# Kernel tuning notes

Measured on AMD Instinct MI355X. Metric: run time of the kernel, lower is better.

## Reference

```python
import jax, jax.numpy as jnp
import numpy as np
from jax import lax

DIM = 192
HEADS = 4
EPS = 1e-12  # torch F.normalize eps


def setup_inputs() -> dict:
    key = jax.random.key(0)
    ks = jax.random.split(key, 8)
    b, c, h, w = 2, DIM, 64, 64
    x = jax.random.normal(ks[0], (b, c, h, w), dtype=jnp.float32)
    # 1x1 qkv conv: weight [3c, c], bias [3c]
    w_qkv = jax.random.normal(ks[1], (3 * c, c), dtype=jnp.float32) * 0.05
    b_qkv = jax.random.normal(ks[2], (3 * c,), dtype=jnp.float32) * 0.05
    # 3x3 depthwise conv (groups = 3c): weight [3c, 1, 3, 3], bias [3c]
    w_dw = jax.random.normal(ks[3], (3 * c, 1, 3, 3), dtype=jnp.float32) * 0.05
    b_dw = jax.random.normal(ks[4], (3 * c,), dtype=jnp.float32) * 0.05
    # 1x1 output projection: weight [c, c], bias [c]
    w_proj = jax.random.normal(ks[5], (c, c), dtype=jnp.float32) * 0.05
    b_proj = jax.random.normal(ks[6], (c,), dtype=jnp.float32) * 0.05
    temperature = jnp.ones((HEADS, 1, 1), dtype=jnp.float32)
    return {"x": x, "w_qkv": w_qkv, "b_qkv": b_qkv, "w_dw": w_dw,
            "b_dw": b_dw, "w_proj": w_proj, "b_proj": b_proj,
            "temperature": temperature}


def _l2norm(t, axis):
    n = jnp.sqrt(jnp.sum(t * t, axis=axis, keepdims=True))
    return t / jnp.maximum(n, EPS)


def reference(x, w_qkv, b_qkv, w_dw, b_dw, w_proj, b_proj, temperature):
    b, c, h, w = x.shape
    heads = temperature.shape[0]
    hd = c // heads  # head dim
    # 1x1 conv -> [b, 3c, h, w]
    qkv = jnp.einsum('bchw,oc->bohw', x, w_qkv) + b_qkv[None, :, None, None]
    # 3x3 depthwise conv, padding 1
    qkv = lax.conv_general_dilated(
        qkv, w_dw, window_strides=(1, 1), padding=((1, 1), (1, 1)),
        dimension_numbers=('NCHW', 'OIHW', 'NCHW'),
        feature_group_count=3 * c) + b_dw[None, :, None, None]
    q, k, v = jnp.split(qkv, 3, axis=1)
    # [b, heads, hd, n] with n = h*w
    q = q.reshape(b, heads, hd, h * w)
    k = k.reshape(b, heads, hd, h * w)
    v = v.reshape(b, heads, hd, h * w)
    q = _l2norm(q, axis=2)
    k = _l2norm(k, axis=2)
    # spatial cosine attention: [b, heads, n, n]
    attn = jnp.einsum('bhdn,bhdm->bhnm', q, k) * temperature[None]
    attn = jax.nn.softmax(attn, axis=-1)
    # out[b,h,d,n] = sum_m attn[n,m] * v[d,m]
    out = jnp.einsum('bhnm,bhdm->bhdn', attn, v)
    out = out.reshape(b, c, h, w)
    out = jnp.einsum('bchw,oc->bohw', out, w_proj) + b_proj[None, :, None, None]
    return out
```

## Files before the change

kernel.cpp:

```cpp
#include <hip/hip_runtime.h>
#include <hip/hip_bf16.h>


#define BB 2
#define CCH 192
#define C3 576
#define NH 4
#define HD 48
#define NP 4096

typedef __hip_bfloat16 bf16;
typedef __attribute__((ext_vector_type(8))) short bf16x8;
typedef __attribute__((ext_vector_type(4))) float f32x4;

union I4B8 { int4 i; bf16x8 v; };

__device__ inline float bf2f(bf16 v){ return __bfloat162float(v); }
__device__ inline unsigned short bfbits(bf16 v){ return __builtin_bit_cast(unsigned short, v); }
__device__ inline unsigned short f2bfbits(float f){ return __builtin_bit_cast(unsigned short, __float2bfloat16(f)); }
__device__ inline float bfb2f(short s){ return __uint_as_float(((unsigned)(unsigned short)s)<<16); }

__global__ void probe_kernel(const unsigned* __restrict__ x, int* __restrict__ flag)
{
  int t = threadIdx.x;
  unsigned u = x[t];
  int e = (u >> 7) & 0xff;
  int sane = (e >= 100 && e <= 140) || ((u & 0x7fffu) == 0u);
  __shared__ int cnt;
  if (t == 0) cnt = 0;
  __syncthreads();
  if (sane) atomicAdd(&cnt, 1);
  __syncthreads();
  if (t == 0) *flag = (cnt >= 192) ? 1 : 0;
}

#define NCANON 153988
__global__ __launch_bounds__(256) void convert_params_kernel(
    const int* __restrict__ flag,
    const void* w_qkv, const void* b_qkv, const void* w_dw, const void* b_dw,
    const void* w_proj, const void* b_proj, const void* temp,
    bf16* __restrict__ canon)
{
  const bool isbf = (*flag != 0);
  int i = blockIdx.x*256 + threadIdx.x;
  if (i >= NCANON) return;
  const void* src; int off;
  if      (i < 110592){ src = w_qkv;  off = i; }
  else if (i < 111168){ src = b_qkv;  off = i - 110592; }
  else if (i < 116352){ src = w_dw;   off = i - 111168; }
  else if (i < 116928){ src = b_dw;   off = i - 116352; }
  else if (i < 153792){ src = w_proj; off = i - 116928; }
  else if (i < 153984){ src = b_proj; off = i - 153792; }
  else                { src = temp;   off = i - 153984; }
  float v = isbf ? bf2f(((const bf16*)src)[off]) : ((const float*)src)[off];
  canon[i] = __float2bfloat16(v);
}

__global__ __launch_bounds__(256) void transpose_x_kernel(
    const int* __restrict__ flag, const void* __restrict__ Xv,
    short* __restrict__ XT)
{
  const bool isbf = (*flag != 0);
  __shared__ short T[64][66];
  const int c0 = blockIdx.x*64, p0 = blockIdx.y*64, b = blockIdx.z;
  const size_t xbase = (size_t)b*CCH*NP;
  #pragma unroll
  for (int s=0;s<16;s++){
    int i = threadIdx.x + s*256;
    int cc = i>>6, pp = i&63;
    size_t g = xbase + (size_t)(c0+cc)*NP + p0+pp;
    float v = isbf ? bf2f(((const bf16*)Xv)[g]) : ((const float*)Xv)[g];
    T[cc][pp] = (short)f2bfbits(v);
  }
  __syncthreads();
  #pragma unroll
  for (int s=0;s<16;s++){
    int i = threadIdx.x + s*256;
    int pl = i>>6, cl = i&63;
    XT[((size_t)b*NP + p0+pl)*CCH + c0+cl] = T[cl][pl];
  }
}

__global__ __launch_bounds__(256) void conv1x1_mfma_kernel(
    const int* __restrict__ flag, int ydyn,
    const short* __restrict__ XT,
    const bf16* __restrict__ Wt,
    const bf16* __restrict__ bias,
    void* __restrict__ Yv, int OC)
{
  const bool yf32 = ydyn && (*flag == 0);
  __shared__ __align__(16) short Bs[2][128*32];
  const int tid = threadIdx.x, wave = tid>>6, lane = tid&63;
  const int l16 = lane&15, quad = lane>>4;
  const int o0 = blockIdx.x*64, p0 = blockIdx.y*128, b = blockIdx.z;
  const short* XTb = XT + ((size_t)b*NP + p0)*CCH;
  const short* Wb  = (const short*)Wt;

  f32x4 acc[4][2];
  #pragma unroll
  for (int mt=0;mt<4;mt++){
    #pragma unroll
    for (int r=0;r<4;r++){
      float bv = bf2f(bias[o0+mt*16+quad*4+r]);
      acc[mt][0][r]=bv; acc[mt][1][r]=bv;
    }
  }

  int4 sreg[2];
  I4B8 Afr[2][4];
  #define CLOAD(kc) { _Pragma("unroll") for (int s_=0;s_<2;s_++){ int i_=tid+256*s_; \
      sreg[s_] = *(const int4*)&XTb[(size_t)(i_>>2)*CCH + (kc)*32 + (i_&3)*8]; } }
  #define CSTORE(buf) { _Pragma("unroll") for (int s_=0;s_<2;s_++){ int i_=tid+256*s_; \
      *(int4*)&Bs[buf][(i_>>2)*32 + (i_&3)*8] = sreg[s_]; } }
  #define ALOAD(kc, buf) { _Pragma("unroll") for (int mt_=0;mt_<4;mt_++){ \
      Afr[buf][mt_].i = *(const int4*)&Wb[(size_t)(o0+mt_*16+l16)*CCH + (kc)*32 + quad*8]; } }

  CLOAD(0); CSTORE(0); ALOAD(0,0);
  __syncthreads();

  #pragma unroll
  for (int kc=0; kc<6; kc++){
    const int cur = kc&1;
    if (kc<5){ CLOAD(kc+1); ALOAD(kc+1, cur^1); }
    I4B8 Bf0, Bf1;
    Bf0.i = *(const int4*)&Bs[cur][(wave*32 + l16)*32 + quad*8];
    Bf1.i = *(const int4*)&Bs[cur][(wave*32 + 16 + l16)*32 + quad*8];
    #pragma unroll
    for (int mt=0;mt<4;mt++){
      acc[mt][0] = __builtin_amdgcn_mfma_f32_16x16x32_bf16(Afr[cur][mt].v, Bf0.v, acc[mt][0], 0,0,0);
      acc[mt][1] = __builtin_amdgcn_mfma_f32_16x16x32_bf16(Afr[cur][mt].v, Bf1.v, acc[mt][1], 0,0,0);
    }
    if (kc<5) CSTORE(cur^1);
    __syncthreads();
  }
  #undef CLOAD
  #undef CSTORE
  #undef ALOAD

  #pragma unroll
  for (int mt=0;mt<4;mt++)
    #pragma unroll
    for (int nt=0;nt<2;nt++)
      #pragma unroll
      for (int r=0;r<4;r++){
        int o = o0 + mt*16 + quad*4 + r;
        int p = p0 + wave*32 + nt*16 + l16;
        size_t off = ((size_t)b*OC + o)*NP + p;
        if (yf32) ((float*)Yv)[off] = acc[mt][nt][r];
        else      ((bf16*)Yv)[off]  = __float2bfloat16(acc[mt][nt][r]);
      }
}

__global__ __launch_bounds__(256) void dwconv_kernel(
    const bf16* __restrict__ in, const bf16* __restrict__ w,
    const bf16* __restrict__ bias, bf16* __restrict__ out)
{
  __shared__ __align__(16) short img[4096];
  const int bc = blockIdx.x; const int ch = bc % C3;
  const int tid = threadIdx.x;
  const int4* g4 = (const int4*)(in + (size_t)bc*NP);
  int4* s4 = (int4*)img;
  s4[tid] = g4[tid];
  s4[tid+256] = g4[tid+256];
  float wv[9];
  #pragma unroll
  for (int j=0;j<9;j++) wv[j] = bf2f(w[ch*9+j]);
  const float bv = bf2f(bias[ch]);
  __syncthreads();

  const int y = tid>>2, x0 = (tid&3)*16;
  unsigned outw[8];
  #pragma unroll
  for (int j=0;j<16;j++){
    int x = x0+j;
    float s = bv;
    #pragma unroll
    for (int ky=0;ky<3;ky++){
      int yy = y+ky-1; if (yy<0||yy>63) continue;
      const short* rp = &img[yy<<6];
      #pragma unroll
      for (int kx=0;kx<3;kx++){
        int xx = x+kx-1; if (xx<0||xx>63) continue;
        s += wv[ky*3+kx]*bfb2f(rp[xx]);
      }
    }
    unsigned hb = f2bfbits(s);
    if (j&1) outw[j>>1] |= hb<<16; else outw[j>>1] = hb;
  }
  int4* op = (int4*)((short*)out + (size_t)bc*NP + (y<<6) + x0);
  op[0] = *(int4*)&outw[0];
  op[1] = *(int4*)&outw[4];
}

__global__ __launch_bounds__(256) void l2norm_t_kernel(
    bf16* __restrict__ buf, short* __restrict__ KT)
{
  int idx = blockIdx.x*256 + threadIdx.x;
  int n = idx & 4095; int t = idx >> 12;
  int head = t & 3; int qk = (t>>2)&1; int b = t>>3;
  bf16* p = buf + ((size_t)b*C3 + qk*CCH + head*HD)*NP + n;
  float v[HD];
  float ss = 0.f;
  #pragma unroll
  for (int d=0; d<HD; d++){ v[d] = bf2f(p[(size_t)d*NP]); ss += v[d]*v[d]; }
  float inv = 1.0f / fmaxf(sqrtf(ss), 1e-12f);
  if (qk == 0){
    #pragma unroll
    for (int d=0; d<HD; d++) p[(size_t)d*NP] = __float2bfloat16(v[d]*inv);
  } else {
    short* row = KT + ((size_t)(b*NH+head)*NP + n)*64;
    int sw = n & 7;
    #pragma unroll
    for (int u=0; u<8; u++){
      int4 w = {0,0,0,0};
      if (u < 6){
        int d0 = u*8;
        w.x = (unsigned)f2bfbits(v[d0+0]*inv) | ((unsigned)f2bfbits(v[d0+1]*inv)<<16);
        w.y = (unsigned)f2bfbits(v[d0+2]*inv) | ((unsigned)f2bfbits(v[d0+3]*inv)<<16);
        w.z = (unsigned)f2bfbits(v[d0+4]*inv) | ((unsigned)f2bfbits(v[d0+5]*inv)<<16);
        w.w = (unsigned)f2bfbits(v[d0+6]*inv) | ((unsigned)f2bfbits(v[d0+7]*inv)<<16);
      }
      *(int4*)&row[(u^sw)*8] = w;
    }
  }
}

__global__ __launch_bounds__(256) void flash_kernel(
    const bf16* __restrict__ qkv,
    const short* __restrict__ KT,
    const bf16* __restrict__ temp,
    short* __restrict__ OT)
{
  __shared__ __align__(16) short Ks[2][128*64];
  __shared__ __align__(16) short Vs[2][48*136];
  __shared__ __align__(16) short Ps[4][16*136];

  const int bh = blockIdx.x, b = bh>>2, head = bh&3;
  const int q0 = blockIdx.y * 64;
  const int tid = threadIdx.x, wave = tid>>6, lane = tid&63;
  const int l16 = lane&15, quad = lane>>4;

  const unsigned short* Qp = (const unsigned short*)(qkv + ((size_t)b*C3 + head*HD)*NP)
                             + q0 + wave*16 + l16;
  const short* Vp = (const short*)(qkv + ((size_t)b*C3 + 2*CCH + head*HD)*NP);
  const short* KTs = KT + (size_t)bh*NP*64;
  const float sc = bf2f(temp[head]) * 1.44269504f;
  const float negM = -__builtin_fabsf(sc);

  I4B8 A0, A1;
  {
    unsigned q0b[8];
    #pragma unroll
    for (int j=0;j<8;j++) q0b[j] = Qp[(size_t)(quad*8+j)*NP];
    A0.i.x = q0b[0] | (q0b[1]<<16); A0.i.y = q0b[2] | (q0b[3]<<16);
    A0.i.z = q0b[4] | (q0b[5]<<16); A0.i.w = q0b[6] | (q0b[7]<<16);
    if (quad < 2){
      unsigned q1b[8];
      #pragma unroll
      for (int j=0;j<8;j++) q1b[j] = Qp[(size_t)(32+quad*8+j)*NP];
      A1.i.x = q1b[0] | (q1b[1]<<16); A1.i.y = q1b[2] | (q1b[3]<<16);
      A1.i.z = q1b[4] | (q1b[5]<<16); A1.i.w = q1b[6] | (q1b[7]<<16);
    } else {
      A1.i.x = 0; A1.i.y = 0; A1.i.z = 0; A1.i.w = 0;
    }
  }

  f32x4 O0 = {0,0,0,0}, O1 = {0,0,0,0}, O2 = {0,0,0,0};
  float rs[4] = {0.f, 0.f, 0.f, 0.f};
  short* Pw = Ps[wave];
  const int sw = l16 & 7;

  int4 kreg[4], vreg[3];
  #define KLOAD(CHUNK) { const int k0_=(CHUNK)<<7; \
    const int4* gk_ = (const int4*)(KTs + (size_t)k0_*64); \
    _Pragma("unroll") for (int s_=0;s_<4;s_++) kreg[s_] = gk_[tid + 256*s_]; \
    _Pragma("unroll") for (int s_=0;s_<3;s_++){ int i_=tid+256*s_; \
      vreg[s_] = *(const int4*)(Vp + (size_t)(i_>>4)*NP + k0_ + (i_&15)*8); } }
  #define KSTORE(BUFI) { int4* lk_ = (int4*)&Ks[BUFI][0]; \
    _Pragma("unroll") for (int s_=0;s_<4;s_++) lk_[tid+256*s_] = kreg[s_]; \
    _Pragma("unroll") for (int s_=0;s_<3;s_++){ int i_=tid+256*s_; \
      *(int4*)&Vs[BUFI][(i_>>4)*136 + (i_&15)*8] = vreg[s_]; } }

  KLOAD(0); KSTORE(0);
  __syncthreads();

  for (int t=0; t<32; ++t){
    const int cur = t & 1;
    if (t < 31) KLOAD(t+1);

    const short* Kb = &Ks[cur][0];
    const short* Vb = &Vs[cur][0];

    f32x4 S[8];
    #pragma unroll
    for (int ct=0; ct<8; ++ct){
      const int row = (ct*16 + l16)*64;
      I4B8 B0, B1;
      B0.i = *(const int4*)&Kb[row + ((quad^sw)*8)];
      B1.i = *(const int4*)&Kb[row + (((4+quad)^sw)*8)];
      f32x4 z = {0,0,0,0};
      z = __builtin_amdgcn_mfma_f32_16x16x32_bf16(A0.v, B0.v, z, 0,0,0);
      z = __builtin_amdgcn_mfma_f32_16x16x32_bf16(A1.v, B1.v, z, 0,0,0);
      S[ct] = z;
    }

    #pragma unroll
    for (int r=0;r<4;r++){
      float acc0 = 0.f, acc1 = 0.f;
      #pragma unroll
      for (int ct=0;ct<8;ct++){
        float p = __builtin_amdgcn_exp2f(__builtin_fmaf(S[ct][r], sc, negM));
        if (ct & 1) acc1 += p; else acc0 += p;
        Pw[(quad*4+r)*136 + ct*16 + l16] = (short)f2bfbits(p);
      }
      rs[r] += acc0 + acc1;
    }

    #pragma unroll
    for (int c=0;c<4;c++){
      I4B8 AP, BV0, BV1, BV2;
      AP.i  = *(const int4*)&Pw[l16*136 + c*32 + quad*8];
      BV0.i = *(const int4*)&Vb[(l16   )*136 + c*32 + quad*8];
      BV1.i = *(const int4*)&Vb[(16+l16)*136 + c*32 + quad*8];
      BV2.i = *(const int4*)&Vb[(32+l16)*136 + c*32 + quad*8];
      O0 = __builtin_amdgcn_mfma_f32_16x16x32_bf16(AP.v, BV0.v, O0, 0,0,0);
      O1 = __builtin_amdgcn_mfma_f32_16x16x32_bf16(AP.v, BV1.v, O1, 0,0,0);
      O2 = __builtin_amdgcn_mfma_f32_16x16x32_bf16(AP.v, BV2.v, O2, 0,0,0);
    }

    if (t < 31) KSTORE(cur^1);
    __syncthreads();
  }
  #undef KLOAD
  #undef KSTORE

  float l[4];
  #pragma unroll
  for (int r=0;r<4;r++){
    float v = rs[r];
    v += __shfl_xor(v,1);
    v += __shfl_xor(v,2);
    v += __shfl_xor(v,4);
    v += __shfl_xor(v,8);
    l[r] = v;
  }

  #pragma unroll
  for (int r=0;r<4;r++){
    float invl = 1.0f / l[r];
    short* row = OT + ((size_t)b*NP + q0 + wave*16 + quad*4 + r)*CCH + head*HD;
    row[l16]    = (short)f2bfbits(O0[r]*invl);
    row[16+l16] = (short)f2bfbits(O1[r]*invl);
    row[32+l16] = (short)f2bfbits(O2[r]*invl);
  }
}

extern "C" void kernel_launch(void* const* d_in, const int* in_sizes, int n_in,
                              void* d_out, int out_size, void* d_ws, size_t ws_size,
                              hipStream_t stream)
{
  int*  flag  = (int*)d_ws;
  bf16* canon = (bf16*)((char*)d_ws + 16);
  bf16* bufA  = (bf16*)((char*)d_ws + 308096);
  bf16* bufB  = (bf16*)((char*)d_ws + 9745280);
  short* XT = (short*)bufB;
  short* OT = (short*)bufA;
  short* KT = (short*)(bufA + 1572864);

  bf16* cw_qkv  = canon;
  bf16* cb_qkv  = canon + 110592;
  bf16* cw_dw   = canon + 111168;
  bf16* cb_dw   = canon + 116352;
  bf16* cw_proj = canon + 116928;
  bf16* cb_proj = canon + 153792;
  bf16* ctemp   = canon + 153984;

  probe_kernel<<<1, 256, 0, stream>>>((const unsigned*)d_in[0], flag);
  convert_params_kernel<<<602, 256, 0, stream>>>(flag,
      d_in[1], d_in[2], d_in[3], d_in[4], d_in[5], d_in[6], d_in[7], canon);
  transpose_x_kernel<<<dim3(3,64,2), 256, 0, stream>>>(flag, d_in[0], XT);
  conv1x1_mfma_kernel<<<dim3(9,32,2), 256, 0, stream>>>(flag, 0,
      XT, cw_qkv, cb_qkv, bufA, C3);
  dwconv_kernel<<<dim3(BB*C3), 256, 0, stream>>>(bufA, cw_dw, cb_dw, bufB);
  l2norm_t_kernel<<<dim3(256), 256, 0, stream>>>(bufB, KT);
  flash_kernel<<<dim3(8,64), 256, 0, stream>>>(bufB, KT, ctemp, OT);
  conv1x1_mfma_kernel<<<dim3(3,32,2), 256, 0, stream>>>(flag, 1,
      OT, cw_proj, cb_proj, d_out, CCH);
}
```

Before: 205.4 us.

## Split attention over key range, keep P in registers, fuse probe into pre-pass

Merges the probe, parameter conversion and x transpose into a single pre-pass kernel that detects the input dtype per block with a wave ballot. The flash kernel is restructured: it computes S transposed (K as A operand), so P stays in registers instead of going through shared memory. It drops double-buffered K/V shared memory, allowing four blocks per CU. When the workspace is large enough it also splits the key range across two blocks and merges fp32 partial outputs and row sums in the projection kernel. This raises the grid from 512 to 1024 blocks to improve occupancy, at the cost of extra fp32 partial-output traffic and added syncs per iteration.

After: 263.9 us. 28.5% more time.

```diff
diff --git a/kernel.cpp b/kernel.cpp
--- a/kernel.cpp
+++ b/kernel.cpp
@@ -19,76 +19,66 @@
 __device__ inline unsigned short bfbits(bf16 v){ return __builtin_bit_cast(unsigned short, v); }
 __device__ inline unsigned short f2bfbits(float f){ return __builtin_bit_cast(unsigned short, __float2bfloat16(f)); }
 __device__ inline float bfb2f(short s){ return __uint_as_float(((unsigned)(unsigned short)s)<<16); }
-
-__global__ void probe_kernel(const unsigned* __restrict__ x, int* __restrict__ flag)
-{
-  int t = threadIdx.x;
-  unsigned u = x[t];
+__device__ inline unsigned pk2(float a, float b){
+  return (unsigned)f2bfbits(a) | ((unsigned)f2bfbits(b)<<16);
+}
+
+__device__ inline bool probe64(const void* x){
+  unsigned u = ((const unsigned*)x)[threadIdx.x & 63];
   int e = (u >> 7) & 0xff;
   int sane = (e >= 100 && e <= 140) || ((u & 0x7fffu) == 0u);
-  __shared__ int cnt;
-  if (t == 0) cnt = 0;
-  __syncthreads();
-  if (sane) atomicAdd(&cnt, 1);
-  __syncthreads();
-  if (t == 0) *flag = (cnt >= 192) ? 1 : 0;
+  unsigned long long m = __ballot(sane);
+  return __popcll(m) >= 48;
 }
 
 #define NCANON 153988
-__global__ __launch_bounds__(256) void convert_params_kernel(
-    const int* __restrict__ flag,
+__global__ __launch_bounds__(256) void pre_kernel(
+    const void* __restrict__ Xv,
     const void* w_qkv, const void* b_qkv, const void* w_dw, const void* b_dw,
     const void* w_proj, const void* b_proj, const void* temp,
-    bf16* __restrict__ canon)
-{
-  const bool isbf = (*flag != 0);
-  int i = blockIdx.x*256 + threadIdx.x;
-  if (i >= NCANON) return;
-  const void* src; int off;
-  if      (i < 110592){ src = w_qkv;  off = i; }
-  else if (i < 111168){ src = b_qkv;  off = i - 110592; }
-  else if (i < 116352){ src = w_dw;   off = i - 111168; }
-  else if (i < 116928){ src = b_dw;   off = i - 116352; }
-  else if (i < 153792){ src = w_proj; off = i - 116928; }
-  else if (i < 153984){ src = b_proj; off = i - 153792; }
-  else                { src = temp;   off = i - 153984; }
-  float v = isbf ? bf2f(((const bf16*)src)[off]) : ((const float*)src)[off];
-  canon[i] = __float2bfloat16(v);
-}
-
-__global__ __launch_bounds__(256) void transpose_x_kernel(
-    const int* __restrict__ flag, const void* __restrict__ Xv,
-    short* __restrict__ XT)
-{
-  const bool isbf = (*flag != 0);
-  __shared__ short T[64][66];
-  const int c0 = blockIdx.x*64, p0 = blockIdx.y*64, b = blockIdx.z;
-  const size_t xbase = (size_t)b*CCH*NP;
-  #pragma unroll
-  for (int s=0;s<16;s++){
-    int i = threadIdx.x + s*256;
-    int cc = i>>6, pp = i&63;
-    size_t g = xbase + (size_t)(c0+cc)*NP + p0+pp;
-    float v = isbf ? bf2f(((const bf16*)Xv)[g]) : ((const float*)Xv)[g];
-    T[cc][pp] = (short)f2bfbits(v);
-  }
-  __syncthreads();
-  #pragma unroll
-  for (int s=0;s<16;s++){
-    int i = threadIdx.x + s*256;
-    int pl = i>>6, cl = i&63;
-    XT[((size_t)b*NP + p0+pl)*CCH + c0+cl] = T[cl][pl];
-  }
-}
-
-__global__ __launch_bounds__(256) void conv1x1_mfma_kernel(
-    const int* __restrict__ flag, int ydyn,
-    const short* __restrict__ XT,
-    const bf16* __restrict__ Wt,
-    const bf16* __restrict__ bias,
-    void* __restrict__ Yv, int OC)
-{
-  const bool yf32 = ydyn && (*flag == 0);
+    bf16* __restrict__ canon, short* __restrict__ XT)
+{
+  const bool isbf = probe64(Xv);
+  const int blk = blockIdx.x;
+  if (blk < 384){
+    __shared__ short T[64][66];
+    const int c0 = (blk % 3)*64, p0 = ((blk/3) % 64)*64, b = blk/192;
+    const size_t xbase = (size_t)b*CCH*NP;
+    #pragma unroll
+    for (int s=0;s<16;s++){
+      int i = threadIdx.x + s*256;
+      int cc = i>>6, pp = i&63;
+      size_t g = xbase + (size_t)(c0+cc)*NP + p0+pp;
+      float v = isbf ? bf2f(((const bf16*)Xv)[g]) : ((const float*)Xv)[g];
+      T[cc][pp] = (short)f2bfbits(v);
+    }
+    __syncthreads();
+    #pragma unroll
+    for (int s=0;s<16;s++){
+      int i = threadIdx.x + s*256;
+      int pl = i>>6, cl = i&63;
+      XT[((size_t)b*NP + p0+pl)*CCH + c0+cl] = T[cl][pl];
+    }
+  } else {
+    int i = (blk-384)*256 + threadIdx.x;
+    if (i >= NCANON) return;
+    const void* src; int off;
+    if      (i < 110592){ src = w_qkv;  off = i; }
+    else if (i < 111168){ src = b_qkv;  off = i - 110592; }
+    else if (i < 116352){ src = w_dw;   off = i - 111168; }
+    else if (i < 116928){ src = b_dw;   off = i - 116352; }
+    else if (i < 153792){ src = w_proj; off = i - 116928; }
+    else if (i < 153984){ src = b_proj; off = i - 153792; }
+    else                { src = temp;   off = i - 153984; }
+    float v = isbf ? bf2f(((const bf16*)src)[off]) : ((const float*)src)[off];
+    canon[i] = __float2bfloat16(v);
+  }
+}
+
+__global__ __launch_bounds__(256) void qkv_conv_kernel(
+    const short* __restrict__ XT, const bf16* __restrict__ Wt,
+    const bf16* __restrict__ bias, bf16* __restrict__ Y)
+{
   __shared__ __align__(16) short Bs[2][128*32];
   const int tid = threadIdx.x, wave = tid>>6, lane = tid&63;
   const int l16 = lane&15, quad = lane>>4;
@@ -105,7 +95,6 @@
       acc[mt][0][r]=bv; acc[mt][1][r]=bv;
     }
   }
-
   int4 sreg[2];
   I4B8 Afr[2][4];
   #define CLOAD(kc) { _Pragma("unroll") for (int s_=0;s_<2;s_++){ int i_=tid+256*s_; \
@@ -114,10 +103,8 @@
       *(int4*)&Bs[buf][(i_>>2)*32 + (i_&3)*8] = sreg[s_]; } }
   #define ALOAD(kc, buf) { _Pragma("unroll") for (int mt_=0;mt_<4;mt_++){ \
       Afr[buf][mt_].i = *(const int4*)&Wb[(size_t)(o0+mt_*16+l16)*CCH + (kc)*32 + quad*8]; } }
-
   CLOAD(0); CSTORE(0); ALOAD(0,0);
   __syncthreads();
-
   #pragma unroll
   for (int kc=0; kc<6; kc++){
     const int cur = kc&1;
@@ -136,7 +123,6 @@
   #undef CLOAD
   #undef CSTORE
   #undef ALOAD
-
   #pragma unroll
   for (int mt=0;mt<4;mt++)
     #pragma unroll
@@ -145,9 +131,7 @@
       for (int r=0;r<4;r++){
         int o = o0 + mt*16 + quad*4 + r;
         int p = p0 + wave*32 + nt*16 + l16;
-        size_t off = ((size_t)b*OC + o)*NP + p;
-        if (yf32) ((float*)Yv)[off] = acc[mt][nt][r];
-        else      ((bf16*)Yv)[off]  = __float2bfloat16(acc[mt][nt][r]);
+        Y[((size_t)b*C3 + o)*NP + p] = __float2bfloat16(acc[mt][nt][r]);
       }
 }
 
@@ -167,7 +151,6 @@
   for (int j=0;j<9;j++) wv[j] = bf2f(w[ch*9+j]);
   const float bv = bf2f(bias[ch]);
   __syncthreads();
-
   const int y = tid>>2, x0 = (tid&3)*16;
   unsigned outw[8];
   #pragma unroll
@@ -215,28 +198,31 @@
       int4 w = {0,0,0,0};
       if (u < 6){
         int d0 = u*8;
-        w.x = (unsigned)f2bfbits(v[d0+0]*inv) | ((unsigned)f2bfbits(v[d0+1]*inv)<<16);
-        w.y = (unsigned)f2bfbits(v[d0+2]*inv) | ((unsigned)f2bfbits(v[d0+3]*inv)<<16);
-        w.z = (unsigned)f2bfbits(v[d0+4]*inv) | ((unsigned)f2bfbits(v[d0+5]*inv)<<16);
-        w.w = (unsigned)f2bfbits(v[d0+6]*inv) | ((unsigned)f2bfbits(v[d0+7]*inv)<<16);
+        w.x = pk2(v[d0+0]*inv, v[d0+1]*inv);
+        w.y = pk2(v[d0+2]*inv, v[d0+3]*inv);
+        w.z = pk2(v[d0+4]*inv, v[d0+5]*inv);
+        w.w = pk2(v[d0+6]*inv, v[d0+7]*inv);
       }
       *(int4*)&row[(u^sw)*8] = w;
     }
   }
 }
 
-__global__ __launch_bounds__(256) void flash_kernel(
+template<int NS>
+__global__ __launch_bounds__(256,4) void flash_kernel(
     const bf16* __restrict__ qkv,
     const short* __restrict__ KT,
     const bf16* __restrict__ temp,
-    short* __restrict__ OT)
-{
-  __shared__ __align__(16) short Ks[2][128*64];
-  __shared__ __align__(16) short Vs[2][48*136];
-  __shared__ __align__(16) short Ps[4][16*136];
+    short* __restrict__ OT,
+    float* __restrict__ Opart,
+    float* __restrict__ lpart)
+{
+  __shared__ __align__(16) short Ks[128*64];
+  __shared__ __align__(16) short Vs[48*136];
 
   const int bh = blockIdx.x, b = bh>>2, head = bh&3;
   const int q0 = blockIdx.y * 64;
+  const int s  = (NS==2) ? blockIdx.z : 0;
   const int tid = threadIdx.x, wave = tid>>6, lane = tid&63;
   const int l16 = lane&15, quad = lane>>4;
 
@@ -247,27 +233,23 @@
   const float sc = bf2f(temp[head]) * 1.44269504f;
   const float negM = -__builtin_fabsf(sc);
 
-  I4B8 A0, A1;
+  I4B8 Q0, Q1;
   {
-    unsigned q0b[8];
-    #pragma unroll
-    for (int j=0;j<8;j++) q0b[j] = Qp[(size_t)(quad*8+j)*NP];
-    A0.i.x = q0b[0] | (q0b[1]<<16); A0.i.y = q0b[2] | (q0b[3]<<16);
-    A0.i.z = q0b[4] | (q0b[5]<<16); A0.i.w = q0b[6] | (q0b[7]<<16);
+    unsigned qb[8];
+    #pragma unroll
+    for (int j=0;j<8;j++) qb[j] = Qp[(size_t)(quad*8+j)*NP];
+    Q0.i.x = qb[0]|(qb[1]<<16); Q0.i.y = qb[2]|(qb[3]<<16);
+    Q0.i.z = qb[4]|(qb[5]<<16); Q0.i.w = qb[6]|(qb[7]<<16);
     if (quad < 2){
-      unsigned q1b[8];
-      #pragma unroll
-      for (int j=0;j<8;j++) q1b[j] = Qp[(size_t)(32+quad*8+j)*NP];
-      A1.i.x = q1b[0] | (q1b[1]<<16); A1.i.y = q1b[2] | (q1b[3]<<16);
-      A1.i.z = q1b[4] | (q1b[5]<<16); A1.i.w = q1b[6] | (q1b[7]<<16);
-    } else {
-      A1.i.x = 0; A1.i.y = 0; A1.i.z = 0; A1.i.w = 0;
-    }
+      #pragma unroll
+      for (int j=0;j<8;j++) qb[j] = Qp[(size_t)(32+quad*8+j)*NP];
+      Q1.i.x = qb[0]|(qb[1]<<16); Q1.i.y = qb[2]|(qb[3]<<16);
+      Q1.i.z = qb[4]|(qb[5]<<16); Q1.i.w = qb[6]|(qb[7]<<16);
+    } else { Q1.i.x=0; Q1.i.y=0; Q1.i.z=0; Q1.i.w=0; }
   }
 
   f32x4 O0 = {0,0,0,0}, O1 = {0,0,0,0}, O2 = {0,0,0,0};
-  float rs[4] = {0.f, 0.f, 0.f, 0.f};
-  short* Pw = Ps[wave];
+  float rs = 0.f;
   const int sw = l16 & 7;
 
   int4 kreg[4], vreg[3];
@@ -276,96 +258,244 @@
     _Pragma("unroll") for (int s_=0;s_<4;s_++) kreg[s_] = gk_[tid + 256*s_]; \
     _Pragma("unroll") for (int s_=0;s_<3;s_++){ int i_=tid+256*s_; \
       vreg[s_] = *(const int4*)(Vp + (size_t)(i_>>4)*NP + k0_ + (i_&15)*8); } }
-  #define KSTORE(BUFI) { int4* lk_ = (int4*)&Ks[BUFI][0]; \
+  #define KSTORE { int4* lk_ = (int4*)Ks; \
     _Pragma("unroll") for (int s_=0;s_<4;s_++) lk_[tid+256*s_] = kreg[s_]; \
     _Pragma("unroll") for (int s_=0;s_<3;s_++){ int i_=tid+256*s_; \
-      *(int4*)&Vs[BUFI][(i_>>4)*136 + (i_&15)*8] = vreg[s_]; } }
-
-  KLOAD(0); KSTORE(0);
+      *(int4*)&Vs[(i_>>4)*136 + (i_&15)*8] = vreg[s_]; } }
+
+  const int t0 = s*(32/NS), tN = t0 + 32/NS;
+  KLOAD(t0); KSTORE;
   __syncthreads();
 
-  for (int t=0; t<32; ++t){
-    const int cur = t & 1;
-    if (t < 31) KLOAD(t+1);
-
-    const short* Kb = &Ks[cur][0];
-    const short* Vb = &Vs[cur][0];
+  for (int t=t0; t<tN; ++t){
+    if (t+1 < tN) KLOAD(t+1);
 
     f32x4 S[8];
     #pragma unroll
     for (int ct=0; ct<8; ++ct){
       const int row = (ct*16 + l16)*64;
-      I4B8 B0, B1;
-      B0.i = *(const int4*)&Kb[row + ((quad^sw)*8)];
-      B1.i = *(const int4*)&Kb[row + (((4+quad)^sw)*8)];
+      I4B8 K0, K1;
+      K0.i = *(const int4*)&Ks[row + ((quad^sw)*8)];
+      K1.i = *(const int4*)&Ks[row + (((4+quad)^sw)*8)];
       f32x4 z = {0,0,0,0};
-      z = __builtin_amdgcn_mfma_f32_16x16x32_bf16(A0.v, B0.v, z, 0,0,0);
-      z = __builtin_amdgcn_mfma_f32_16x16x32_bf16(A1.v, B1.v, z, 0,0,0);
+      z = __builtin_amdgcn_mfma_f32_16x16x32_bf16(K0.v, Q0.v, z, 0,0,0);
+      z = __builtin_amdgcn_mfma_f32_16x16x32_bf16(K1.v, Q1.v, z, 0,0,0);
       S[ct] = z;
     }
 
-    #pragma unroll
-    for (int r=0;r<4;r++){
-      float acc0 = 0.f, acc1 = 0.f;
-      #pragma unroll
-      for (int ct=0;ct<8;ct++){
-        float p = __builtin_amdgcn_exp2f(__builtin_fmaf(S[ct][r], sc, negM));
-        if (ct & 1) acc1 += p; else acc0 += p;
-        Pw[(quad*4+r)*136 + ct*16 + l16] = (short)f2bfbits(p);
-      }
-      rs[r] += acc0 + acc1;
-    }
-
+    I4B8 Pf[4];
     #pragma unroll
     for (int c=0;c<4;c++){
-      I4B8 AP, BV0, BV1, BV2;
-      AP.i  = *(const int4*)&Pw[l16*136 + c*32 + quad*8];
-      BV0.i = *(const int4*)&Vb[(l16   )*136 + c*32 + quad*8];
-      BV1.i = *(const int4*)&Vb[(16+l16)*136 + c*32 + quad*8];
-      BV2.i = *(const int4*)&Vb[(32+l16)*136 + c*32 + quad*8];
-      O0 = __builtin_amdgcn_mfma_f32_16x16x32_bf16(AP.v, BV0.v, O0, 0,0,0);
-      O1 = __builtin_amdgcn_mfma_f32_16x16x32_bf16(AP.v, BV1.v, O1, 0,0,0);
-      O2 = __builtin_amdgcn_mfma_f32_16x16x32_bf16(AP.v, BV2.v, O2, 0,0,0);
-    }
-
-    if (t < 31) KSTORE(cur^1);
-    __syncthreads();
+      float pa[4], pb[4];
+      #pragma unroll
+      for (int r=0;r<4;r++){
+        pa[r] = __builtin_amdgcn_exp2f(__builtin_fmaf(S[2*c][r],   sc, negM));
+        pb[r] = __builtin_amdgcn_exp2f(__builtin_fmaf(S[2*c+1][r], sc, negM));
+      }
+      rs += (pa[0]+pa[1]) + (pa[2]+pa[3]) + (pb[0]+pb[1]) + (pb[2]+pb[3]);
+      Pf[c].i.x = pk2(pa[0],pa[1]); Pf[c].i.y = pk2(pa[2],pa[3]);
+      Pf[c].i.z = pk2(pb[0],pb[1]); Pf[c].i.w = pk2(pb[2],pb[3]);
+    }
+
+    #pragma unroll
+    for (int c=0;c<4;c++){
+      #pragma unroll
+      for (int mt=0;mt<3;mt++){
+        I4B8 Vf;
+        int2 v0 = *(const int2*)&Vs[(mt*16+l16)*136 + c*32 + quad*4];
+        int2 v1 = *(const int2*)&Vs[(mt*16+l16)*136 + c*32 + 16 + quad*4];
+        Vf.i.x = v0.x; Vf.i.y = v0.y; Vf.i.z = v1.x; Vf.i.w = v1.y;
+        if (mt==0) O0 = __builtin_amdgcn_mfma_f32_16x16x32_bf16(Vf.v, Pf[c].v, O0, 0,0,0);
+        if (mt==1) O1 = __builtin_amdgcn_mfma_f32_16x16x32_bf16(Vf.v, Pf[c].v, O1, 0,0,0);
+        if (mt==2) O2 = __builtin_amdgcn_mfma_f32_16x16x32_bf16(Vf.v, Pf[c].v, O2, 0,0,0);
+      }
+    }
+
+    if (t+1 < tN){
+      __syncthreads();
+      KSTORE;
+      __syncthreads();
+    }
   }
   #undef KLOAD
   #undef KSTORE
 
-  float l[4];
-  #pragma unroll
-  for (int r=0;r<4;r++){
-    float v = rs[r];
-    v += __shfl_xor(v,1);
-    v += __shfl_xor(v,2);
-    v += __shfl_xor(v,4);
-    v += __shfl_xor(v,8);
-    l[r] = v;
-  }
-
-  #pragma unroll
-  for (int r=0;r<4;r++){
-    float invl = 1.0f / l[r];
-    short* row = OT + ((size_t)b*NP + q0 + wave*16 + quad*4 + r)*CCH + head*HD;
-    row[l16]    = (short)f2bfbits(O0[r]*invl);
-    row[16+l16] = (short)f2bfbits(O1[r]*invl);
-    row[32+l16] = (short)f2bfbits(O2[r]*invl);
-  }
+  rs += __shfl_xor(rs, 16);
+  rs += __shfl_xor(rs, 32);
+
+  const int n = q0 + wave*16 + l16;
+  if (NS == 1){
+    float invl = 1.0f / rs;
+    short* row = OT + ((size_t)b*NP + n)*CCH + head*HD;
+    unsigned u0, u1;
+    u0 = pk2(O0[0]*invl, O0[1]*invl); u1 = pk2(O0[2]*invl, O0[3]*invl);
+    { int2 w = {(int)u0,(int)u1}; *(int2*)&row[quad*4] = w; }
+    u0 = pk2(O1[0]*invl, O1[1]*invl); u1 = pk2(O1[2]*invl, O1[3]*invl);
+    { int2 w = {(int)u0,(int)u1}; *(int2*)&row[16+quad*4] = w; }
+    u0 = pk2(O2[0]*invl, O2[1]*invl); u1 = pk2(O2[2]*invl, O2[3]*invl);
+    { int2 w = {(int)u0,(int)u1}; *(int2*)&row[32+quad*4] = w; }
+  } else {
+    float* Ob = Opart + (((size_t)s*BB + b)*NP + n)*CCH + head*HD;
+    *(f32x4*)&Ob[quad*4]      = O0;
+    *(f32x4*)&Ob[16+quad*4]   = O1;
+    *(f32x4*)&Ob[32+quad*4]   = O2;
+    if (quad == 0) lpart[((size_t)s*8 + bh)*NP + n] = rs;
+  }
+}
+
+__global__ __launch_bounds__(256) void proj_split_kernel(
+    const void* __restrict__ Xprobe,
+    const float* __restrict__ Opart, const float* __restrict__ lpart,
+    const bf16* __restrict__ Wt, const bf16* __restrict__ bias,
+    void* __restrict__ Yv)
+{
+  const bool yf32 = !probe64(Xprobe);
+  __shared__ __align__(16) short Bs[2][128*32];
+  const int tid = threadIdx.x, wave = tid>>6, lane = tid&63;
+  const int l16 = lane&15, quad = lane>>4;
+  const int o0 = blockIdx.x*64, p0 = blockIdx.y*128, b = blockIdx.z;
+  const short* Wb = (const short*)Wt;
+  const float* Oa = Opart + ((size_t)b*NP + p0)*CCH;
+  const float* Obp = Opart + (((size_t)BB + b)*NP + p0)*CCH;
+
+  f32x4 acc[4][2];
+  #pragma unroll
+  for (int mt=0;mt<4;mt++){
+    #pragma unroll
+    for (int r=0;r<4;r++){
+      float bv = bf2f(bias[o0+mt*16+quad*4+r]);
+      acc[mt][0][r]=bv; acc[mt][1][r]=bv;
+    }
+  }
+  int4 sreg[2];
+  I4B8 Afr[2][4];
+  #define CLOAD(kc) { _Pragma("unroll") for (int s_=0;s_<2;s_++){ int i_=tid+256*s_; \
+      int p_=i_>>2, c8_=(kc)*32+(i_&3)*8; int hd_=c8_/48; \
+      float l_ = lpart[((size_t)(b*4+hd_))*NP + p0+p_] \
+               + lpart[((size_t)(8+b*4+hd_))*NP + p0+p_]; \
+      float inv_ = 1.0f/l_; \
+      const float* a_ = Oa  + (size_t)p_*CCH + c8_; \
+      const float* b_ = Obp + (size_t)p_*CCH + c8_; \
+      f32x4 x0_=*(const f32x4*)a_, x1_=*(const f32x4*)(a_+4); \
+      f32x4 y0_=*(const f32x4*)b_, y1_=*(const f32x4*)(b_+4); \
+      sreg[s_].x = (int)pk2((x0_[0]+y0_[0])*inv_, (x0_[1]+y0_[1])*inv_); \
+      sreg[s_].y = (int)pk2((x0_[2]+y0_[2])*inv_, (x0_[3]+y0_[3])*inv_); \
+      sreg[s_].z = (int)pk2((x1_[0]+y1_[0])*inv_, (x1_[1]+y1_[1])*inv_); \
+      sreg[s_].w = (int)pk2((x1_[2]+y1_[2])*inv_, (x1_[3]+y1_[3])*inv_); } }
+  #define CSTORE(buf) { _Pragma("unroll") for (int s_=0;s_<2;s_++){ int i_=tid+256*s_; \
+      *(int4*)&Bs[buf][(i_>>2)*32 + (i_&3)*8] = sreg[s_]; } }
+  #define ALOAD(kc, buf) { _Pragma("unroll") for (int mt_=0;mt_<4;mt_++){ \
+      Afr[buf][mt_].i = *(const int4*)&Wb[(size_t)(o0+mt_*16+l16)*CCH + (kc)*32 + quad*8]; } }
+  CLOAD(0); CSTORE(0); ALOAD(0,0);
+  __syncthreads();
+  #pragma unroll
+  for (int kc=0; kc<6; kc++){
+    const int cur = kc&1;
+    if (kc<5){ CLOAD(kc+1); ALOAD(kc+1, cur^1); }
+    I4B8 Bf0, Bf1;
+    Bf0.i = *(const int4*)&Bs[cur][(wave*32 + l16)*32 + quad*8];
+    Bf1.i = *(const int4*)&Bs[cur][(wave*32 + 16 + l16)*32 + quad*8];
+    #pragma unroll
+    for (int mt=0;mt<4;mt++){
+      acc[mt][0] = __builtin_amdgcn_mfma_f32_16x16x32_bf16(Afr[cur][mt].v, Bf0.v, acc[mt][0], 0,0,0);
+      acc[mt][1] = __builtin_amdgcn_mfma_f32_16x16x32_bf16(Afr[cur][mt].v, Bf1.v, acc[mt][1], 0,0,0);
+    }
+    if (kc<5) CSTORE(cur^1);
+    __syncthreads();
+  }
+  #undef CLOAD
+  #undef CSTORE
+  #undef ALOAD
+  #pragma unroll
+  for (int mt=0;mt<4;mt++)
+    #pragma unroll
+    for (int nt=0;nt<2;nt++)
+      #pragma unroll
+      for (int r=0;r<4;r++){
+        int o = o0 + mt*16 + quad*4 + r;
+        int p = p0 + wave*32 + nt*16 + l16;
+        size_t off = ((size_t)b*CCH + o)*NP + p;
+        if (yf32) ((float*)Yv)[off] = acc[mt][nt][r];
+        else      ((bf16*)Yv)[off]  = __float2bfloat16(acc[mt][nt][r]);
+      }
+}
+
+__global__ __launch_bounds__(256) void proj_nosplit_kernel(
+    const void* __restrict__ Xprobe,
+    const short* __restrict__ OT, const bf16* __restrict__ Wt,
+    const bf16* __restrict__ bias, void* __restrict__ Yv)
+{
+  const bool yf32 = !probe64(Xprobe);
+  __shared__ __align__(16) short Bs[2][128*32];
+  const int tid = threadIdx.x, wave = tid>>6, lane = tid&63;
+  const int l16 = lane&15, quad = lane>>4;
+  const int o0 = blockIdx.x*64, p0 = blockIdx.y*128, b = blockIdx.z;
+  const short* XTb = OT + ((size_t)b*NP + p0)*CCH;
+  const short* Wb  = (const short*)Wt;
+  f32x4 acc[4][2];
+  #pragma unroll
+  for (int mt=0;mt<4;mt++){
+    #pragma unroll
+    for (int r=0;r<4;r++){
+      float bv = bf2f(bias[o0+mt*16+quad*4+r]);
+      acc[mt][0][r]=bv; acc[mt][1][r]=bv;
+    }
+  }
+  int4 sreg[2];
+  I4B8 Afr[2][4];
+  #define CLOAD(kc) { _Pragma("unroll") for (int s_=0;s_<2;s_++){ int i_=tid+256*s_; \
+      sreg[s_] = *(const int4*)&XTb[(size_t)(i_>>2)*CCH + (kc)*32 + (i_&3)*8]; } }
+  #define CSTORE(buf) { _Pragma("unroll") for (int s_=0;s_<2;s_++){ int i_=tid+256*s_; \
+      *(int4*)&Bs[buf][(i_>>2)*32 + (i_&3)*8] = sreg[s_]; } }
+  #define ALOAD(kc, buf) { _Pragma("unroll") for (int mt_=0;mt_<4;mt_++){ \
+      Afr[buf][mt_].i = *(const int4*)&Wb[(size_t)(o0+mt_*16+l16)*CCH + (kc)*32 + quad*8]; } }
+  CLOAD(0); CSTORE(0); ALOAD(0,0);
+  __syncthreads();
+  #pragma unroll
+  for (int kc=0; kc<6; kc++){
+    const int cur = kc&1;
+    if (kc<5){ CLOAD(kc+1); ALOAD(kc+1, cur^1); }
+    I4B8 Bf0, Bf1;
+    Bf0.i = *(const int4*)&Bs[cur][(wave*32 + l16)*32 + quad*8];
+    Bf1.i = *(const int4*)&Bs[cur][(wave*32 + 16 + l16)*32 + quad*8];
+    #pragma unroll
+    for (int mt=0;mt<4;mt++){
+      acc[mt][0] = __builtin_amdgcn_mfma_f32_16x16x32_bf16(Afr[cur][mt].v, Bf0.v, acc[mt][0], 0,0,0);
+      acc[mt][1] = __builtin_amdgcn_mfma_f32_16x16x32_bf16(Afr[cur][mt].v, Bf1.v, acc[mt][1], 0,0,0);
+    }
+    if (kc<5) CSTORE(cur^1);
+    __syncthreads();
+  }
+  #undef CLOAD
+  #undef CSTORE
+  #undef ALOAD
+  #pragma unroll
+  for (int mt=0;mt<4;mt++)
+    #pragma unroll
+    for (int nt=0;nt<2;nt++)
+      #pragma unroll
+      for (int r=0;r<4;r++){
+        int o = o0 + mt*16 + quad*4 + r;
+        int p = p0 + wave*32 + nt*16 + l16;
+        size_t off = ((size_t)b*CCH + o)*NP + p;
+        if (yf32) ((float*)Yv)[off] = acc[mt][nt][r];
+        else      ((bf16*)Yv)[off]  = __float2bfloat16(acc[mt][nt][r]);
+      }
 }
 
 extern "C" void kernel_launch(void* const* d_in, const int* in_sizes, int n_in,
                               void* d_out, int out_size, void* d_ws, size_t ws_size,
                               hipStream_t stream)
 {
-  int*  flag  = (int*)d_ws;
   bf16* canon = (bf16*)((char*)d_ws + 16);
   bf16* bufA  = (bf16*)((char*)d_ws + 308096);
   bf16* bufB  = (bf16*)((char*)d_ws + 9745280);
   short* XT = (short*)bufB;
   short* OT = (short*)bufA;
   short* KT = (short*)(bufA + 1572864);
+  float* Opart = (float*)((char*)d_ws + 19182464);
+  float* lpart = (float*)((char*)d_ws + 31765376);
+  const bool split = (ws_size >= 32027520ull);
 
   bf16* cw_qkv  = canon;
   bf16* cb_qkv  = canon + 110592;
@@ -375,15 +505,21 @@
   bf16* cb_proj = canon + 153792;
   bf16* ctemp   = canon + 153984;
 
-  probe_kernel<<<1, 256, 0, stream>>>((const unsigned*)d_in[0], flag);
-  convert_params_kernel<<<602, 256, 0, stream>>>(flag,
-      d_in[1], d_in[2], d_in[3], d_in[4], d_in[5], d_in[6], d_in[7], canon);
-  transpose_x_kernel<<<dim3(3,64,2), 256, 0, stream>>>(flag, d_in[0], XT);
-  conv1x1_mfma_kernel<<<dim3(9,32,2), 256, 0, stream>>>(flag, 0,
-      XT, cw_qkv, cb_qkv, bufA, C3);
+  pre_kernel<<<986, 256, 0, stream>>>(d_in[0],
+      d_in[1], d_in[2], d_in[3], d_in[4], d_in[5], d_in[6], d_in[7],
+      canon, XT);
+  qkv_conv_kernel<<<dim3(9,32,2), 256, 0, stream>>>(XT, cw_qkv, cb_qkv, bufA);
   dwconv_kernel<<<dim3(BB*C3), 256, 0, stream>>>(bufA, cw_dw, cb_dw, bufB);
   l2norm_t_kernel<<<dim3(256), 256, 0, stream>>>(bufB, KT);
-  flash_kernel<<<dim3(8,64), 256, 0, stream>>>(bufB, KT, ctemp, OT);
-  conv1x1_mfma_kernel<<<dim3(3,32,2), 256, 0, stream>>>(flag, 1,
-      OT, cw_proj, cb_proj, d_out, CCH);
-}
+  if (split){
+    flash_kernel<2><<<dim3(8,64,2), 256, 0, stream>>>(bufB, KT, ctemp,
+        (short*)nullptr, Opart, lpart);
+    proj_split_kernel<<<dim3(3,32,2), 256, 0, stream>>>(d_in[0],
+        Opart, lpart, cw_proj, cb_proj, d_out);
+  } else {
+    flash_kernel<1><<<dim3(8,64,1), 256, 0, stream>>>(bufB, KT, ctemp,
+        OT, (float*)nullptr, (float*)nullptr);
+    proj_nosplit_kernel<<<dim3(3,32,2), 256, 0, stream>>>(d_in[0],
+        OT, cw_proj, cb_proj, d_out);
+  }
+}
```
